# Kernel tuning notes

Hardware: AMD Instinct MI355X
Metric: run time of the kernel (lower is better)

The kernel has to match this reference:

```python
import jax, jax.numpy as jnp
import numpy as np

B, U = 64, 512          # batch, max_units
CORE, UNIT = 512, 256   # core_output_size, unit_embedding_size
HID, ACT = 1024, 12     # hidden_layer_size, ACTION_COUNT


def setup_inputs() -> dict:
    key = jax.random.key(0)
    ks = jax.random.split(key, 6)
    core_output = jax.random.normal(ks[0], (B, 1, CORE), dtype=jnp.float32)
    own_unit_embeddings = jax.random.normal(ks[1], (B, U, UNIT), dtype=jnp.float32)
    nr_units = jax.random.randint(ks[2], (B, 1), 0, U, dtype=jnp.int32)
    nr_own_flags = jax.random.randint(ks[3], (B, 1), 0, 64, dtype=jnp.int32)
    W1 = jax.random.normal(ks[4], (CORE + UNIT, HID), dtype=jnp.float32) * (1.0 / np.sqrt(CORE + UNIT))
    b1 = jnp.zeros((HID,), dtype=jnp.float32)
    W2 = jax.random.normal(ks[5], (HID, ACT), dtype=jnp.float32) * (1.0 / np.sqrt(HID))
    b2 = jnp.zeros((ACT,), dtype=jnp.float32)
    return {"core_output": core_output, "own_unit_embeddings": own_unit_embeddings,
            "nr_units": nr_units, "nr_own_flags": nr_own_flags,
            "W1": W1, "b1": b1, "W2": W2, "b2": b2}


def reference(core_output, own_unit_embeddings, nr_units, nr_own_flags, W1, b1, W2, b2):
    b, u, _ = own_unit_embeddings.shape
    # broadcast core output to every unit slot and concat along features: [B, U, UNIT+CORE]
    core_rep = jnp.broadcast_to(core_output, (b, u, core_output.shape[-1]))
    combined = jnp.concatenate([own_unit_embeddings, core_rep], axis=-1)
    autoregressive_embedding = jax.nn.relu(jnp.einsum('buf,fh->buh', combined, W1) + b1)
    logits = jnp.einsum('buh,ha->bua', autoregressive_embedding, W2) + b2
    action_probs = jax.nn.softmax(logits, axis=-1)
    # vectorized range mask: mask[i, f:n, :] = 1 else 1e-9
    idx = jnp.arange(u, dtype=nr_units.dtype)[None, :]        # [1, U]
    valid = (idx >= nr_own_flags) & (idx < nr_units)          # [B, U]
    mask = jnp.where(valid, 1.0, 1e-9).astype(action_probs.dtype)[:, :, None]
    return action_probs * mask, autoregressive_embedding
```

## Files before the change

### kernel.cpp

```cpp
#include <hip/hip_runtime.h>
#include <hip/hip_fp16.h>
#include <cstdint>

typedef unsigned short ushort_t;
typedef _Float16 f16x8 __attribute__((ext_vector_type(8)));
typedef float f32x4 __attribute__((ext_vector_type(4)));
typedef unsigned int u32x4 __attribute__((ext_vector_type(4)));

#define M_TOT  32768
#define K_EMB  256
#define K_CORE 512
#define ACT    12

__device__ __forceinline__ unsigned int pack2h(float a, float b) {
    __half2 h = __floats2half2_rn(a, b);
    union { __half2 h2; unsigned int u; } v; v.h2 = h; return v.u;
}

__global__ __launch_bounds__(1024) void prep_k(const float* __restrict__ W1,
                                               ushort_t* __restrict__ W1T,
                                               const float* __restrict__ core,
                                               const float* __restrict__ b1,
                                               float* __restrict__ cp) {
    __shared__ float tile[64][65];
    __shared__ float part[3][256];
    const int id = blockIdx.x;
    const int t = threadIdx.x;
    if (id < 64) {
        const int k0 = (id & 3) * 64, n0 = (id >> 2) * 64;
        const int r = t >> 4, c4 = (t & 15) * 4;
        const float4 v = *(const float4*)(W1 + (size_t)(k0 + r) * 1024 + n0 + c4);
        tile[r][c4 + 0] = v.x; tile[r][c4 + 1] = v.y;
        tile[r][c4 + 2] = v.z; tile[r][c4 + 3] = v.w;
        __syncthreads();
        uint2 o;
        o.x = pack2h(tile[c4 + 0][r], tile[c4 + 1][r]);
        o.y = pack2h(tile[c4 + 2][r], tile[c4 + 3][r]);
        const int n  = n0 + r;
        const int kk = k0 + c4;
        const int it   = ((n >> 7) << 3) + (kk >> 5);
        const int rgrp = (n >> 4) & 7;
        const int lane = (((kk >> 3) & 3) << 4) + (n & 15);
        const size_t addr = (size_t)it * 4096 + rgrp * 512 + lane * 8 + (kk & 7);
        *(uint2*)(W1T + addr) = o;
    } else {
        const int xb = id - 64;
        const int b = xb >> 2;
        const int nl = t & 255;
        const int n = (xb & 3) * 256 + nl;
        const int kq = t >> 8;
        const float* cr = core + (size_t)b * K_CORE + kq * 128;
        const float* wp = W1 + (size_t)(K_EMB + kq * 128) * 1024 + n;
        float s0 = 0.f, s1 = 0.f, s2 = 0.f, s3 = 0.f;
#pragma unroll 8
        for (int k = 0; k < 128; k += 4) {
            s0 += cr[k + 0] * wp[(size_t)(k + 0) * 1024];
            s1 += cr[k + 1] * wp[(size_t)(k + 1) * 1024];
            s2 += cr[k + 2] * wp[(size_t)(k + 2) * 1024];
            s3 += cr[k + 3] * wp[(size_t)(k + 3) * 1024];
        }
        const float s = (s0 + s1) + (s2 + s3);
        if (kq) part[kq - 1][nl] = s;
        __syncthreads();
        if (kq == 0)
            cp[b * 1024 + n] = b1[n] + s + part[0][nl] + part[1][nl] + part[2][nl];
    }
}

__global__ __launch_bounds__(256, 4) void fused_k(const float* __restrict__ emb,
                                                  const ushort_t* __restrict__ w1t,
                                                  const float* __restrict__ cp,
                                                  const float* __restrict__ W2,
                                                  const float* __restrict__ b2,
                                                  const int* __restrict__ nr_units,
                                                  const int* __restrict__ nr_flags,
                                                  float* __restrict__ out0,
                                                  float* __restrict__ out1) {
    __shared__ __align__(16) ushort_t Asl[32 * 256];
    __shared__ __align__(16) float logitP[4][32][ACT];

    const int t = threadIdx.x;
    const int w = t >> 6, L = t & 63;
    const int lane16 = L & 15, qd = L >> 4;
    const int m0 = blockIdx.x * 32;
    const int bb = blockIdx.x >> 4;

    {
        const int g = t & 31;
        const int r0 = t >> 5;
#pragma unroll
        for (int p = 0; p < 4; ++p) {
            const int r = p * 8 + r0;
            const float* src = emb + (size_t)(m0 + r) * K_EMB + g * 8;
            const f32x4 v0 = __builtin_nontemporal_load((const f32x4*)src);
            const f32x4 v1 = __builtin_nontemporal_load((const f32x4*)src + 1);
            u32x4 pk;
            pk[0] = pack2h(v0[0], v0[1]); pk[1] = pack2h(v0[2], v0[3]);
            pk[2] = pack2h(v1[0], v1[1]); pk[3] = pack2h(v1[2], v1[3]);
            *(u32x4*)((char*)Asl + r * 512 + ((g ^ (r & 7)) << 4)) = pk;
        }
    }
    __syncthreads();

    const int araw0 = lane16 * 512;
    const int araw1 = (16 + lane16) * 512;
    const int axor = lane16 & 7;

    f32x4 la[2][3];
#pragma unroll
    for (int mi = 0; mi < 2; ++mi)
#pragma unroll
        for (int c = 0; c < 3; ++c) la[mi][c] = (f32x4){0.f, 0.f, 0.f, 0.f};

#pragma unroll
    for (int nc = 0; nc < 8; ++nc) {
        f32x4 acc[2][2];
#pragma unroll
        for (int ni = 0; ni < 2; ++ni)
#pragma unroll
            for (int mi = 0; mi < 2; ++mi) acc[ni][mi] = (f32x4){0.f, 0.f, 0.f, 0.f};

        const ushort_t* sb = w1t + (size_t)(w * 2 + (nc >> 2)) * 8 * 4096
                                 + ((nc & 3) * 2) * 512 + L * 8;
#pragma unroll
        for (int ks = 0; ks < 8; ++ks) {
            const f16x8 bf0 = *(const f16x8*)(sb + ks * 4096);
            const f16x8 bf1 = *(const f16x8*)(sb + ks * 4096 + 512);
            const int ga = (((ks << 2) | qd) ^ axor) << 4;
            const f16x8 af0 = *(const f16x8*)((const char*)Asl + araw0 + ga);
            const f16x8 af1 = *(const f16x8*)((const char*)Asl + araw1 + ga);
            acc[0][0] = __builtin_amdgcn_mfma_f32_16x16x32_f16(bf0, af0, acc[0][0], 0, 0, 0);
            acc[0][1] = __builtin_amdgcn_mfma_f32_16x16x32_f16(bf0, af1, acc[0][1], 0, 0, 0);
            acc[1][0] = __builtin_amdgcn_mfma_f32_16x16x32_f16(bf1, af0, acc[1][0], 0, 0, 0);
            acc[1][1] = __builtin_amdgcn_mfma_f32_16x16x32_f16(bf1, af1, acc[1][1], 0, 0, 0);
        }

#pragma unroll
        for (int ni = 0; ni < 2; ++ni) {
            const int nbase = w * 256 + nc * 32 + ni * 16 + qd * 4;
            const f32x4 cpv = *(const f32x4*)(cp + bb * 1024 + nbase);
#pragma unroll
            for (int mi = 0; mi < 2; ++mi) {
                f32x4 v = acc[ni][mi] + cpv;
#pragma unroll
                for (int j = 0; j < 4; ++j) v[j] = v[j] > 0.f ? v[j] : 0.f;
                acc[ni][mi] = v;
                const size_t m = (size_t)(m0 + mi * 16 + lane16);
                __builtin_nontemporal_store(v, (f32x4*)(out1 + m * 1024 + nbase));
            }
#pragma unroll
            for (int r = 0; r < 4; ++r) {
                const f32x4* wp = (const f32x4*)(W2 + (size_t)(nbase + r) * ACT);
                const f32x4 w2a = wp[0], w2b = wp[1], w2c = wp[2];
#pragma unroll
                for (int mi = 0; mi < 2; ++mi) {
                    const float vv = acc[ni][mi][r];
                    la[mi][0] += w2a * vv;
                    la[mi][1] += w2b * vv;
                    la[mi][2] += w2c * vv;
                }
            }
        }
    }

#pragma unroll
    for (int mi = 0; mi < 2; ++mi)
#pragma unroll
        for (int c = 0; c < 3; ++c)
#pragma unroll
            for (int j = 0; j < 4; ++j) {
                la[mi][c][j] += __shfl_xor(la[mi][c][j], 16, 64);
                la[mi][c][j] += __shfl_xor(la[mi][c][j], 32, 64);
            }
    if (qd == 0) {
#pragma unroll
        for (int mi = 0; mi < 2; ++mi) {
            f32x4* p = (f32x4*)&logitP[w][mi * 16 + lane16][0];
            p[0] = la[mi][0]; p[1] = la[mi][1]; p[2] = la[mi][2];
        }
    }
    __syncthreads();

    if (t < 32) {
        float lg[ACT];
#pragma unroll
        for (int a = 0; a < ACT; ++a)
            lg[a] = logitP[0][t][a] + logitP[1][t][a]
                  + logitP[2][t][a] + logitP[3][t][a] + b2[a];
        float mx = lg[0];
#pragma unroll
        for (int a = 1; a < ACT; ++a) mx = fmaxf(mx, lg[a]);
        float s = 0.f;
#pragma unroll
        for (int a = 0; a < ACT; ++a) { lg[a] = __expf(lg[a] - mx); s += lg[a]; }
        const float inv = 1.f / s;
        const int m = m0 + t;
        const int u = m & 511;
        const float msk = (u >= nr_flags[bb] && u < nr_units[bb]) ? 1.0f : 1e-9f;
        f32x4 o0, o1, o2;
#pragma unroll
        for (int j = 0; j < 4; ++j) {
            o0[j] = lg[j] * inv * msk;
            o1[j] = lg[j + 4] * inv * msk;
            o2[j] = lg[j + 8] * inv * msk;
        }
        f32x4* op = (f32x4*)(out0 + (size_t)m * ACT);
        __builtin_nontemporal_store(o0, op + 0);
        __builtin_nontemporal_store(o1, op + 1);
        __builtin_nontemporal_store(o2, op + 2);
    }
}

extern "C" void kernel_launch(void* const* d_in, const int* in_sizes, int n_in,
                              void* d_out, int out_size, void* d_ws, size_t ws_size,
                              hipStream_t stream) {
    const float* core   = (const float*)d_in[0];
    const float* emb    = (const float*)d_in[1];
    const int* nr_units = (const int*)d_in[2];
    const int* nr_flags = (const int*)d_in[3];
    const float* W1     = (const float*)d_in[4];
    const float* b1     = (const float*)d_in[5];
    const float* W2     = (const float*)d_in[6];
    const float* b2     = (const float*)d_in[7];

    float* out0 = (float*)d_out;
    float* out1 = out0 + (size_t)M_TOT * ACT;

    ushort_t* w1t = (ushort_t*)d_ws;
    float* cp = (float*)((char*)d_ws + (size_t)1024 * 256 * 2);

    prep_k<<<dim3(320), 1024, 0, stream>>>(W1, w1t, core, b1, cp);
    fused_k<<<dim3(1024), 256, 0, stream>>>(emb, w1t, cp, W2, b2, nr_units, nr_flags, out0, out1);
}
```

Before: 245.6 us.

## Stage hidden activations through LDS for coalesced row-contiguous output stores

Each wave now owns a 32-column slice of every 128-column chunk instead of a contiguous 256-column band. The ReLU'd hidden tile is written into a double-buffered, XOR-swizzled LDS stage and then read back so each half-wave stores 512 contiguous bytes of a row to the large embedding output. Before, each store instruction scattered 64-byte pieces across 16 rows. The cost is an extra LDS round trip, a block barrier per chunk, and 32KB more shared memory, which lowers the occupancy hint from 4 to 3 blocks per CU. The logit partial buffer is aliased onto the stage buffer.

```diff
diff --git a/kernel.cpp b/kernel.cpp
--- a/kernel.cpp
+++ b/kernel.cpp
@@ -67,7 +67,7 @@
     }
 }
 
-__global__ __launch_bounds__(256, 4) void fused_k(const float* __restrict__ emb,
+__global__ __launch_bounds__(256, 3) void fused_k(const float* __restrict__ emb,
                                                   const ushort_t* __restrict__ w1t,
                                                   const float* __restrict__ cp,
                                                   const float* __restrict__ W2,
@@ -77,7 +77,8 @@
                                                   float* __restrict__ out0,
                                                   float* __restrict__ out1) {
     __shared__ __align__(16) ushort_t Asl[32 * 256];
-    __shared__ __align__(16) float logitP[4][32][ACT];
+    __shared__ __align__(16) float hstage[2][32][128];
+    float* logitP = (float*)&hstage[0][0][0];
 
     const int t = threadIdx.x;
     const int w = t >> 6, L = t & 63;
@@ -120,8 +121,7 @@
 #pragma unroll
             for (int mi = 0; mi < 2; ++mi) acc[ni][mi] = (f32x4){0.f, 0.f, 0.f, 0.f};
 
-        const ushort_t* sb = w1t + (size_t)(w * 2 + (nc >> 2)) * 8 * 4096
-                                 + ((nc & 3) * 2) * 512 + L * 8;
+        const ushort_t* sb = w1t + (size_t)nc * 8 * 4096 + (w * 2) * 512 + L * 8;
 #pragma unroll
         for (int ks = 0; ks < 8; ++ks) {
             const f16x8 bf0 = *(const f16x8*)(sb + ks * 4096);
@@ -135,19 +135,26 @@
             acc[1][1] = __builtin_amdgcn_mfma_f32_16x16x32_f16(bf1, af1, acc[1][1], 0, 0, 0);
         }
 
+        char* hb = (char*)&hstage[nc & 1][0][0];
 #pragma unroll
         for (int ni = 0; ni < 2; ++ni) {
-            const int nbase = w * 256 + nc * 32 + ni * 16 + qd * 4;
+            const int nbase = nc * 128 + w * 32 + ni * 16 + qd * 4;
             const f32x4 cpv = *(const f32x4*)(cp + bb * 1024 + nbase);
+            const int c4 = w * 8 + ni * 4 + qd;
 #pragma unroll
             for (int mi = 0; mi < 2; ++mi) {
                 f32x4 v = acc[ni][mi] + cpv;
 #pragma unroll
                 for (int j = 0; j < 4; ++j) v[j] = v[j] > 0.f ? v[j] : 0.f;
                 acc[ni][mi] = v;
-                const size_t m = (size_t)(m0 + mi * 16 + lane16);
-                __builtin_nontemporal_store(v, (f32x4*)(out1 + m * 1024 + nbase));
-            }
+                const int row = mi * 16 + lane16;
+                *(f32x4*)(hb + row * 512 + ((c4 ^ (row & 7)) << 4)) = v;
+            }
+        }
+
+#pragma unroll
+        for (int ni = 0; ni < 2; ++ni) {
+            const int nbase = nc * 128 + w * 32 + ni * 16 + qd * 4;
 #pragma unroll
             for (int r = 0; r < 4; ++r) {
                 const f32x4* wp = (const f32x4*)(W2 + (size_t)(nbase + r) * ACT);
@@ -161,6 +168,19 @@
                 }
             }
         }
+
+        __syncthreads();
+
+        {
+            const int f = L & 31, rh = L >> 5;
+#pragma unroll
+            for (int i = 0; i < 4; ++i) {
+                const int row = w * 8 + i * 2 + rh;
+                const f32x4 v = *(const f32x4*)(hb + row * 512 + ((f ^ (row & 7)) << 4));
+                __builtin_nontemporal_store(v,
+                    (f32x4*)(out1 + (size_t)(m0 + row) * 1024 + nc * 128 + f * 4));
+            }
+        }
     }
 
 #pragma unroll
@@ -175,7 +195,7 @@
     if (qd == 0) {
 #pragma unroll
         for (int mi = 0; mi < 2; ++mi) {
-            f32x4* p = (f32x4*)&logitP[w][mi * 16 + lane16][0];
+            f32x4* p = (f32x4*)&logitP[(w * 32 + mi * 16 + lane16) * ACT];
             p[0] = la[mi][0]; p[1] = la[mi][1]; p[2] = la[mi][2];
         }
     }
@@ -185,8 +205,8 @@
         float lg[ACT];
 #pragma unroll
         for (int a = 0; a < ACT; ++a)
-            lg[a] = logitP[0][t][a] + logitP[1][t][a]
-                  + logitP[2][t][a] + logitP[3][t][a] + b2[a];
+            lg[a] = logitP[(0 * 32 + t) * ACT + a] + logitP[(1 * 32 + t) * ACT + a]
+                  + logitP[(2 * 32 + t) * ACT + a] + logitP[(3 * 32 + t) * ACT + a] + b2[a];
         float mx = lg[0];
 #pragma unroll
         for (int a = 1; a < ACT; ++a) mx = fmaxf(mx, lg[a]);
```

Measured after the change: 250.8 us. +2.1%, slower.
